# Kernel optimization log

Hardware: AMD Instinct MI355X
Metric: run time of the kernel (lower is better)

## Reference

```python
import jax, jax.numpy as jnp
import numpy as np

HEADS = 8
NEG_SLOPE = 0.2


def _gat_conv(x, src, dst, W, a_src, a_dst, b, heads, ch):
    # PyG GATConv (v1), eval mode (dropout inactive), add_self_loops=True, concat=True.
    N = x.shape[0]
    loop = jnp.arange(N)
    s = jnp.concatenate([src, loop])
    d = jnp.concatenate([dst, loop])
    h = (x @ W).reshape(N, heads, ch)                      # [N, H, C]
    alpha_src = jnp.einsum('nhc,hc->nh', h, a_src)          # [N, H]
    alpha_dst = jnp.einsum('nhc,hc->nh', h, a_dst)
    e = jax.nn.leaky_relu(alpha_src[s] + alpha_dst[d], NEG_SLOPE)  # [E, H]
    m = jax.ops.segment_max(e, d, num_segments=N)           # segment softmax over dst
    ex = jnp.exp(e - m[d])
    denom = jax.ops.segment_sum(ex, d, num_segments=N)
    alpha = ex / (denom[d] + 1e-16)
    out = jax.ops.segment_sum(h[s] * alpha[:, :, None], d, num_segments=N)  # [N, H, C]
    return out.reshape(N, heads * ch) + b


def setup_inputs() -> dict:
    key = jax.random.key(0)
    ks = jax.random.split(key, 20)
    B, N, F_in = 8, 1024, 16
    E = 131072
    C1, C2 = 8, 128                     # per-head channels of conv1 / conv2
    D = N * HEADS * C2                  # flattened head input = 1024*1024
    NA, AC = 4, 4                       # len(num_actions)=4, each 4 actions

    def w(k, shape, fan_in):
        return jax.random.normal(k, shape, jnp.float32) * (1.0 / np.sqrt(fan_in))

    inp = {
        'x': jax.random.normal(ks[0], (B, N, F_in), jnp.float32),
        'edge': jax.random.randint(ks[1], (2, E), 0, B * N, jnp.int64),
        'W1': w(ks[2], (F_in, HEADS * C1), F_in),
        'a_src1': w(ks[3], (HEADS, C1), C1),
        'a_dst1': w(ks[4], (HEADS, C1), C1),
        'b1': jnp.zeros((HEADS * C1,), jnp.float32),
        'W2': w(ks[5], (HEADS * C1, HEADS * C2), HEADS * C1),
        'a_src2': w(ks[6], (HEADS, C2), C2),
        'a_dst2': w(ks[7], (HEADS, C2), C2),
        'b2': jnp.zeros((HEADS * C2,), jnp.float32),
        'adv_w': w(ks[8], (D, NA * AC), D),
        'adv_b': jnp.zeros((NA * AC,), jnp.float32),
        'val1_w': w(ks[9], (D, 64), D),
        'val1_b': jnp.zeros((64,), jnp.float32),
        'val2_w': w(ks[10], (64, 64), 64),
        'val2_b': jnp.zeros((64,), jnp.float32),
        'val3_w': w(ks[11], (64, 1), 64),
        'val3_b': jnp.zeros((1,), jnp.float32),
    }
    return inp


def reference(x, edge, W1, a_src1, a_dst1, b1, W2, a_src2, a_dst2, b2,
              adv_w, adv_b, val1_w, val1_b, val2_w, val2_b, val3_w, val3_b):
    B, N, F_in = x.shape
    src, dst = edge[0], edge[1]
    h = x.reshape(B * N, F_in)
    h = jax.nn.relu(_gat_conv(h, src, dst, W1, a_src1, a_dst1, b1, HEADS, 8))
    h = jax.nn.relu(_gat_conv(h, src, dst, W2, a_src2, a_dst2, b2, HEADS, 128))
    h = h.reshape(B, -1)                                   # [B, N*1024]
    adv = jax.nn.relu(h @ adv_w + adv_b).reshape(B, 4, 4)  # [B, len(num_actions), actions]
    v = jax.nn.relu(h @ val1_w + val1_b)
    v = jax.nn.relu(v @ val2_w + val2_b)
    v = v @ val3_w + val3_b                                # [B, 1]
    return v[:, :, None] + adv - adv.mean(-1, keepdims=True)
```

## Files before the change

kernel.cpp:

```cpp
#include <hip/hip_runtime.h>
#include <stdint.h>

#define NODES   8192
#define BATCH   8
#define FIN     16
#define HC1     64
#define HC2     1024
#define DTOT    1048576
#define NEG     0.2f

typedef unsigned short u16;

__device__ __forceinline__ float b2f(u16 s){ return __uint_as_float(((unsigned)s)<<16); }
__device__ __forceinline__ u16 f2b(float f){
    unsigned u = __float_as_uint(f);
    unsigned r = u + 0x7fffu + ((u>>16)&1u);
    return (u16)(r>>16);
}
__device__ __forceinline__ float lrelu(float x){ return x > 0.f ? x : NEG*x; }
__device__ __forceinline__ float ldf(const void* p, long i, int isf){
    return isf ? ((const float*)p)[i] : b2f(((const u16*)p)[i]);
}

__device__ __forceinline__ int esrc(const int* e, int i, int i64){ return i64 ? e[2*i] : e[i]; }
__device__ __forceinline__ int edst(const int* e, int i, int E, int i64){ return i64 ? e[2*(E+i)] : e[E+i]; }

__global__ __launch_bounds__(256) void k_prep(const u16* __restrict__ xs, const int* __restrict__ ed,
        int* flags, int* counts){
    int t = threadIdx.x;
    if(blockIdx.x == 0){
        __shared__ int cnt[2];
        if(t<2) cnt[t]=0;
        __syncthreads();
        int bad=0;
        for(int i=t;i<1024;i+=256){
            u16 u = xs[i];
            float a = fabsf(b2f(u));
            if(!(u==0 || (a>1e-8f && a<1e4f))) bad++;
        }
        if(bad) atomicAdd(&cnt[0], bad);
        int z=0;
        for(int i=t;i<1024;i+=256){
            if(ed[2*i+1]==0) z++;
        }
        if(z) atomicAdd(&cnt[1], z);
        __syncthreads();
        if(t==0){ flags[0] = (cnt[0] > 64) ? 1 : 0; flags[1] = (cnt[1] > 512) ? 1 : 0; }
    } else {
        int i = (blockIdx.x-1)*256 + t;
        if(i < NODES) counts[i] = 0;
    }
}

__global__ __launch_bounds__(256) void k_cnt_d1(const int* __restrict__ ed, int E, int* counts,
        const void* __restrict__ x, const void* __restrict__ W1,
        const void* __restrict__ asw, const void* __restrict__ adw,
        float* g1, float* as1, float* ad1, const int* flags){
    int t = threadIdx.x;
    if(blockIdx.x < 512){
        int i64 = flags[1];
        int e = blockIdx.x*256 + t;
        if(e < E) atomicAdd(&counts[edst(ed,e,E,i64)], 1);
        return;
    }
    int isf = flags[0];
    __shared__ float w1[FIN*HC1];
    __shared__ float av[64], dv[64];
    __shared__ float xr[4][FIN];
    __shared__ float hrow[4][HC1];
    int n0 = (blockIdx.x-512)*4;
    for(int i=t;i<FIN*HC1;i+=256) w1[i] = ldf(W1,i,isf);
    if(t<64){ av[t]=ldf(asw,t,isf); dv[t]=ldf(adw,t,isf); }
    if(t<64) xr[t>>4][t&15] = ldf(x, n0*FIN + t, isf);
    __syncthreads();
    int i = t>>6, c = t&63;
    float acc = 0.f;
    #pragma unroll
    for(int k=0;k<FIN;k++) acc += xr[i][k]*w1[k*HC1+c];
    g1[(n0+i)*HC1 + c] = acc;
    hrow[i][c] = acc;
    __syncthreads();
    if(t<32){
        int ii=t>>3, h=t&7;
        float sa=0.f, sd=0.f;
        #pragma unroll
        for(int k=0;k<8;k++){ float v=hrow[ii][h*8+k]; sa+=v*av[h*8+k]; sd+=v*dv[h*8+k]; }
        as1[(n0+ii)*8+h]=sa; ad1[(n0+ii)*8+h]=sd;
    }
}

__global__ __launch_bounds__(1024) void k_scan(const int* __restrict__ counts, int* offs, int* cursor){
    __shared__ int sums[1024];
    int t = threadIdx.x;
    int base = t*8;
    int loc[8]; int s = 0;
    for(int k=0;k<8;k++){ loc[k] = s; s += counts[base+k]; }
    sums[t] = s;
    __syncthreads();
    for(int off=1; off<1024; off<<=1){
        int v = (t>=off) ? sums[t-off] : 0;
        __syncthreads();
        sums[t] += v;
        __syncthreads();
    }
    int b = (t==0) ? 0 : sums[t-1];
    for(int k=0;k<8;k++){ int v = b + loc[k]; offs[base+k]=v; cursor[base+k]=v; }
    if(t==1023) offs[NODES] = sums[1023];
}

__global__ void k_fill(const int* __restrict__ ed, int E, int* cursor, int* csr, const int* flags){
    int i64 = flags[1];
    int e = blockIdx.x*256 + threadIdx.x;
    if(e < E){ int p = atomicAdd(&cursor[edst(ed,e,E,i64)], 1); csr[p] = esrc(ed,e,i64); }
}

__global__ __launch_bounds__(64) void k_agg1(const int* __restrict__ offs, const int* __restrict__ csr,
        const float* __restrict__ g1, const float* __restrict__ as1, const float* __restrict__ ad1,
        const void* __restrict__ b1, float* z1, const int* flags){
    int isf = flags[0];
    __shared__ float redm[64], redd[64];
    __shared__ float mh[8], dh[8], adl[8];
    __shared__ int src_l[64];
    __shared__ float wx[64*8];
    int n = blockIdx.x, t = threadIdx.x;
    int off = offs[n], deg = offs[n+1]-off, tot = deg+1;
    if(t<8) adl[t] = ad1[n*8+t];
    __syncthreads();
    {
        int h = t&7, jg = t>>3;
        float ad = adl[h];
        float m = -1e30f, d = 0.f;
        for(int j=jg; j<tot; j+=8){
            int s = (j<deg)?csr[off+j]:n;
            float e = lrelu(as1[s*8+h] + ad);
            if(e>m){ d = d*__expf(m-e) + 1.f; m = e; } else d += __expf(e-m);
        }
        redm[t]=m; redd[t]=d;
        __syncthreads();
        for(int st=4; st>=1; st>>=1){
            if(jg < st){
                float m2 = redm[t + st*8], d2 = redd[t + st*8];
                float mm = fmaxf(m, m2);
                d = d*__expf(m-mm) + d2*__expf(m2-mm);
                m = mm;
                redm[t]=m; redd[t]=d;
            }
            __syncthreads();
        }
        if(t<8){ mh[t]=redm[t]; dh[t]=redd[t] + 1e-16f; }
        __syncthreads();
    }
    int c = t, hc = t>>3;
    float acc = 0.f;
    for(int c0=0;c0<tot;c0+=64){
        int nc = min(64, tot-c0);
        if(t<nc){ int j=c0+t; src_l[t]=(j<deg)?csr[off+j]:n; }
        __syncthreads();
        for(int p=t;p<nc*8;p+=64){
            int j=p>>3, hh=p&7;
            float e = lrelu(as1[src_l[j]*8+hh] + adl[hh]);
            wx[p] = __expf(e - mh[hh]);
        }
        __syncthreads();
        int j = 0;
        for(; j+2<=nc; j+=2){
            float w0 = wx[j*8+hc],     v0 = g1[src_l[j]*HC1 + c];
            float w1 = wx[(j+1)*8+hc], v1 = g1[src_l[j+1]*HC1 + c];
            acc += w0*v0 + w1*v1;
        }
        if(j<nc) acc += wx[j*8+hc]*g1[src_l[j]*HC1 + c];
        __syncthreads();
    }
    z1[n*HC1 + c] = fmaxf(acc/dh[hc] + ldf(b1,c,isf), 0.f);
}

__global__ __launch_bounds__(256) void k_d2a2(const float* __restrict__ z1,
        const void* __restrict__ W2, const void* __restrict__ asw, const void* __restrict__ adw,
        u16* g2, float* as2, float* ad2, const int* flags){
    int isf = flags[0];
    __shared__ float zr[8][HC1];
    __shared__ float avs[HC2], ads[HC2];
    int t = threadIdx.x;
    int n0 = blockIdx.x*8;
    for(int i=t;i<8*HC1;i+=256) zr[i>>6][i&63] = z1[n0*HC1 + i];
    for(int i=t;i<HC2;i+=256){ avs[i]=ldf(asw,i,isf); ads[i]=ldf(adw,i,isf); }
    __syncthreads();
    int c0 = t*4;
    float acc[8][4];
    #pragma unroll
    for(int i=0;i<8;i++){ acc[i][0]=0;acc[i][1]=0;acc[i][2]=0;acc[i][3]=0; }
    for(int k=0;k<HC1;k++){
        float w0,w1,w2,w3;
        if(isf){
            float4 w = *(const float4*)((const float*)W2 + (size_t)k*HC2 + c0);
            w0=w.x; w1=w.y; w2=w.z; w3=w.w;
        } else {
            ushort4 w = *(const ushort4*)((const u16*)W2 + (size_t)k*HC2 + c0);
            w0=b2f(w.x); w1=b2f(w.y); w2=b2f(w.z); w3=b2f(w.w);
        }
        #pragma unroll
        for(int i=0;i<8;i++){
            float zv = zr[i][k];
            acc[i][0]+=zv*w0; acc[i][1]+=zv*w1; acc[i][2]+=zv*w2; acc[i][3]+=zv*w3;
        }
    }
    float a0=avs[c0], a1=avs[c0+1], a2=avs[c0+2], a3=avs[c0+3];
    float d0=ads[c0], d1=ads[c0+1], d2=ads[c0+2], d3=ads[c0+3];
    int h = t>>5;
    #pragma unroll
    for(int i=0;i<8;i++){
        ushort4 o;
        o.x=f2b(acc[i][0]); o.y=f2b(acc[i][1]); o.z=f2b(acc[i][2]); o.w=f2b(acc[i][3]);
        *(ushort4*)&g2[(size_t)(n0+i)*HC2 + c0] = o;
        float pa = acc[i][0]*a0 + acc[i][1]*a1 + acc[i][2]*a2 + acc[i][3]*a3;
        float pd = acc[i][0]*d0 + acc[i][1]*d1 + acc[i][2]*d2 + acc[i][3]*d3;
        #pragma unroll
        for(int m=1;m<32;m<<=1){ pa += __shfl_xor(pa,m); pd += __shfl_xor(pd,m); }
        if((t&31)==0){ as2[(n0+i)*8+h]=pa; ad2[(n0+i)*8+h]=pd; }
    }
}

__global__ __launch_bounds__(256) void k_agg2(const int* __restrict__ offs, const int* __restrict__ csr,
        const u16* __restrict__ g2, const float* __restrict__ as2, const float* __restrict__ ad2,
        const void* __restrict__ b2, u16* hbf, const int* flags){
    int isf = flags[0];
    __shared__ float redm[256], redd[256];
    __shared__ float mh[8], dh[8], adl[8];
    __shared__ int src_l[64];
    __shared__ float wx[64*8];
    int n = blockIdx.x, t = threadIdx.x;
    int off = offs[n], deg = offs[n+1]-off, tot = deg+1;
    if(t<8) adl[t] = ad2[n*8+t];
    __syncthreads();
    {
        int h = t&7, jg = t>>3;
        float ad = adl[h];
        float m = -1e30f, d = 0.f;
        for(int j=jg; j<tot; j+=32){
            int s = (j<deg)?csr[off+j]:n;
            float e = lrelu(as2[s*8+h] + ad);
            if(e>m){ d = d*__expf(m-e) + 1.f; m = e; } else d += __expf(e-m);
        }
        redm[t]=m; redd[t]=d;
        __syncthreads();
        for(int st=16; st>=1; st>>=1){
            if(jg < st){
                float m2 = redm[t + st*8], d2 = redd[t + st*8];
                float mm = fmaxf(m, m2);
                d = d*__expf(m-mm) + d2*__expf(m2-mm);
                m = mm;
                redm[t]=m; redd[t]=d;
            }
            __syncthreads();
        }
        if(t<8){ mh[t]=redm[t]; dh[t]=redd[t] + 1e-16f; }
        __syncthreads();
    }
    int c0 = t*4, hc = t>>5;
    float acc[4] = {0,0,0,0};
    for(int cc0=0;cc0<tot;cc0+=64){
        int nc = min(64, tot-cc0);
        if(t<nc){ int j=cc0+t; src_l[t]=(j<deg)?csr[off+j]:n; }
        __syncthreads();
        for(int p=t;p<nc*8;p+=256){
            int j=p>>3, hh=p&7;
            float e = lrelu(as2[src_l[j]*8+hh] + adl[hh]);
            wx[p] = __expf(e - mh[hh]);
        }
        __syncthreads();
        int j = 0;
        for(; j+2<=nc; j+=2){
            float w0 = wx[j*8+hc], w1 = wx[(j+1)*8+hc];
            ushort4 gv0 = *(const ushort4*)&g2[(size_t)src_l[j]*HC2 + c0];
            ushort4 gv1 = *(const ushort4*)&g2[(size_t)src_l[j+1]*HC2 + c0];
            acc[0]+=w0*b2f(gv0.x)+w1*b2f(gv1.x);
            acc[1]+=w0*b2f(gv0.y)+w1*b2f(gv1.y);
            acc[2]+=w0*b2f(gv0.z)+w1*b2f(gv1.z);
            acc[3]+=w0*b2f(gv0.w)+w1*b2f(gv1.w);
        }
        if(j<nc){
            float w = wx[j*8+hc];
            ushort4 gv = *(const ushort4*)&g2[(size_t)src_l[j]*HC2 + c0];
            acc[0]+=w*b2f(gv.x); acc[1]+=w*b2f(gv.y); acc[2]+=w*b2f(gv.z); acc[3]+=w*b2f(gv.w);
        }
        __syncthreads();
    }
    float dhv = dh[hc];
    ushort4 o;
    o.x = f2b(fmaxf(acc[0]/dhv + ldf(b2,c0+0,isf), 0.f));
    o.y = f2b(fmaxf(acc[1]/dhv + ldf(b2,c0+1,isf), 0.f));
    o.z = f2b(fmaxf(acc[2]/dhv + ldf(b2,c0+2,isf), 0.f));
    o.w = f2b(fmaxf(acc[3]/dhv + ldf(b2,c0+3,isf), 0.f));
    *(ushort4*)&hbf[(size_t)n*HC2 + c0] = o;
}

template<int COLS, int NW>
__device__ __forceinline__ void gemv_part(const void* __restrict__ W, const u16* __restrict__ hbf,
        float* __restrict__ scratch, int wid, int lane, int isf){
    const int GR    = COLS/8;
    const int KSTEP = 64/GR;
    const int ITERS = DTOT/(NW*KSTEP);
    int cg  = (lane % GR)*8;
    int kof = lane / GR;
    float acc[8][8];
    #pragma unroll
    for(int b=0;b<8;b++)
        #pragma unroll
        for(int c=0;c<8;c++) acc[b][c]=0.f;
    for(int it=0; it<ITERS; it+=2){
        int k0 = (it*NW + wid)*KSTEP + kof;
        int k1 = ((it+1)*NW + wid)*KSTEP + kof;
        float wv0[8], wv1[8];
        if(isf){
            float4 a0 = *(const float4*)((const float*)W + (size_t)k0*COLS + cg);
            float4 b0 = *(const float4*)((const float*)W + (size_t)k0*COLS + cg + 4);
            float4 a1 = *(const float4*)((const float*)W + (size_t)k1*COLS + cg);
            float4 b1 = *(const float4*)((const float*)W + (size_t)k1*COLS + cg + 4);
            wv0[0]=a0.x;wv0[1]=a0.y;wv0[2]=a0.z;wv0[3]=a0.w;wv0[4]=b0.x;wv0[5]=b0.y;wv0[6]=b0.z;wv0[7]=b0.w;
            wv1[0]=a1.x;wv1[1]=a1.y;wv1[2]=a1.z;wv1[3]=a1.w;wv1[4]=b1.x;wv1[5]=b1.y;wv1[6]=b1.z;wv1[7]=b1.w;
        } else {
            ushort4 a0 = *(const ushort4*)((const u16*)W + (size_t)k0*COLS + cg);
            ushort4 b0 = *(const ushort4*)((const u16*)W + (size_t)k0*COLS + cg + 4);
            ushort4 a1 = *(const ushort4*)((const u16*)W + (size_t)k1*COLS + cg);
            ushort4 b1 = *(const ushort4*)((const u16*)W + (size_t)k1*COLS + cg + 4);
            wv0[0]=b2f(a0.x);wv0[1]=b2f(a0.y);wv0[2]=b2f(a0.z);wv0[3]=b2f(a0.w);
            wv0[4]=b2f(b0.x);wv0[5]=b2f(b0.y);wv0[6]=b2f(b0.z);wv0[7]=b2f(b0.w);
            wv1[0]=b2f(a1.x);wv1[1]=b2f(a1.y);wv1[2]=b2f(a1.z);wv1[3]=b2f(a1.w);
            wv1[4]=b2f(b1.x);wv1[5]=b2f(b1.y);wv1[6]=b2f(b1.z);wv1[7]=b2f(b1.w);
        }
        float hv0[8], hv1[8];
        #pragma unroll
        for(int b=0;b<8;b++){ hv0[b] = b2f(hbf[(size_t)b*DTOT + k0]); hv1[b] = b2f(hbf[(size_t)b*DTOT + k1]); }
        #pragma unroll
        for(int b=0;b<8;b++)
            #pragma unroll
            for(int c=0;c<8;c++) acc[b][c] += hv0[b]*wv0[c] + hv1[b]*wv1[c];
    }
    #pragma unroll
    for(int m=GR;m<64;m<<=1){
        #pragma unroll
        for(int b=0;b<8;b++)
            #pragma unroll
            for(int c=0;c<8;c++) acc[b][c] += __shfl_xor(acc[b][c], m);
    }
    int q = lane / GR;
    if(q < 8){
        float4 o0, o1;
        o0.x=acc[q][0]; o0.y=acc[q][1]; o0.z=acc[q][2]; o0.w=acc[q][3];
        o1.x=acc[q][4]; o1.y=acc[q][5]; o1.z=acc[q][6]; o1.w=acc[q][7];
        float* dst = scratch + (size_t)wid*COLS*8 + q*COLS + cg;
        *(float4*)dst       = o0;
        *(float4*)(dst + 4) = o1;
    }
}

__global__ __launch_bounds__(256) void k_heads(const void* __restrict__ v1w, const void* __restrict__ advw,
        const u16* __restrict__ hbf, float* s1, float* s2, const int* flags){
    int isf = flags[0];
    int lane = threadIdx.x & 63;
    if(blockIdx.x < 1024){
        int wid = (int)((blockIdx.x*256 + threadIdx.x) >> 6);
        gemv_part<64,4096>(v1w, hbf, s1, wid, lane, isf);
    } else {
        int wid = (int)(((blockIdx.x-1024)*256 + threadIdx.x) >> 6);
        gemv_part<16,1024>(advw, hbf, s2, wid, lane, isf);
    }
}

__global__ __launch_bounds__(1024) void k_reduce(const float* __restrict__ s1, const float* __restrict__ s2,
        float* v1a, float* adva){
    __shared__ float red[1024];
    int blk = blockIdx.x, t = threadIdx.x;
    int ph = t>>6, ln = t&63;
    float a = 0.f;
    if(blk < 8){
        int o = blk*64 + ln;
        for(int p = ph; p < 4096; p += 16) a += s1[(size_t)p*512 + o];
        red[t] = a; __syncthreads();
        if(t<64){ float s=0.f; for(int q=0;q<16;q++) s += red[q*64+t]; v1a[blk*64+t]=s; }
    } else {
        int o = (blk-8)*64 + ln;
        for(int p = ph; p < 1024; p += 16) a += s2[(size_t)p*128 + o];
        red[t] = a; __syncthreads();
        if(t<64){ float s=0.f; for(int q=0;q<16;q++) s += red[q*64+t]; adva[(blk-8)*64+t]=s; }
    }
}

__global__ __launch_bounds__(512) void k_final(const float* __restrict__ v1a, const float* __restrict__ adva,
        const void* __restrict__ v1b, const void* __restrict__ advb,
        const void* __restrict__ w2v, const void* __restrict__ b2v,
        const void* __restrict__ w3v, const void* __restrict__ b3v,
        void* out, const int* flags){
    int isf = flags[0];
    __shared__ float v1[8][64], v2[8][64], adv[128], v3[8];
    int t = threadIdx.x;
    { int b=t>>6, j=t&63; v1[b][j] = fmaxf(v1a[t] + ldf(v1b,j,isf), 0.f); }
    if(t<128) adv[t] = fmaxf(adva[t] + ldf(advb,t&15,isf), 0.f);
    __syncthreads();
    { int b=t>>6, j=t&63;
      float a=0.f;
      for(int k=0;k<64;k++) a += v1[b][k]*ldf(w2v,k*64+j,isf);
      v2[b][j] = fmaxf(a + ldf(b2v,j,isf), 0.f); }
    __syncthreads();
    if(t<8){
        float a=0.f;
        for(int k=0;k<64;k++) a += v2[t][k]*ldf(w3v,k,isf);
        v3[t] = a + ldf(b3v,0,isf);
    }
    __syncthreads();
    if(t<128){
        int b=t>>4, r=(t>>2)&3;
        int base = b*16 + r*4;
        float m = 0.25f*(adv[base]+adv[base+1]+adv[base+2]+adv[base+3]);
        float val = v3[b] + adv[t] - m;
        if(isf) ((float*)out)[t] = val;
        else    ((u16*)out)[t]   = f2b(val);
    }
}

extern "C" void kernel_launch(void* const* d_in, const int* in_sizes, int n_in,
                              void* d_out, int out_size, void* d_ws, size_t ws_size,
                              hipStream_t stream){
    const void* x    = d_in[0];
    const int*  edge = (const int*)d_in[1];
    const int E = in_sizes[1]/2;
    const void* W1   = d_in[2];
    const void* as1w = d_in[3];
    const void* ad1w = d_in[4];
    const void* b1   = d_in[5];
    const void* W2   = d_in[6];
    const void* as2w = d_in[7];
    const void* ad2w = d_in[8];
    const void* b2   = d_in[9];
    const void* advw = d_in[10];
    const void* advb = d_in[11];
    const void* v1w  = d_in[12];
    const void* v1b  = d_in[13];
    const void* v2w  = d_in[14];
    const void* v2b  = d_in[15];
    const void* v3w  = d_in[16];
    const void* v3b  = d_in[17];

    char* wsp = (char*)d_ws;
    size_t o = 0;
    auto alloc = [&](size_t bytes)->char*{
        char* p = wsp + o;
        o = (o + bytes + 255) & ~(size_t)255;
        return p;
    };
    int*   flags  = (int*)  alloc(256);
    int*   counts = (int*)  alloc(NODES*4);
    int*   offs   = (int*)  alloc((NODES+8)*4);
    int*   cursor = (int*)  alloc(NODES*4);
    int*   csr    = (int*)  alloc((size_t)E*4);
    float* g1     = (float*)alloc((size_t)NODES*HC1*4);
    float* as1    = (float*)alloc((size_t)NODES*8*4);
    float* ad1    = (float*)alloc((size_t)NODES*8*4);
    float* z1     = (float*)alloc((size_t)NODES*HC1*4);
    u16*   g2     = (u16*)  alloc((size_t)NODES*HC2*2);
    float* as2    = (float*)alloc((size_t)NODES*8*4);
    float* ad2    = (float*)alloc((size_t)NODES*8*4);
    u16*   hbf    = (u16*)  alloc((size_t)NODES*HC2*2);
    float* s1     = (float*)alloc((size_t)4096*512*4);
    float* s2     = (float*)alloc((size_t)1024*128*4);
    float* v1a    = (float*)alloc(512*4);
    float* adva   = (float*)alloc(128*4);

    k_prep  <<<33, 256, 0, stream>>>((const u16*)x, edge, flags, counts);
    k_cnt_d1<<<2560, 256, 0, stream>>>(edge, E, counts, x, W1, as1w, ad1w, g1, as1, ad1, flags);
    k_scan  <<<1, 1024, 0, stream>>>(counts, offs, cursor);
    k_fill  <<<(E+255)/256, 256, 0, stream>>>(edge, E, cursor, csr, flags);
    k_agg1  <<<NODES, 64, 0, stream>>>(offs, csr, g1, as1, ad1, b1, z1, flags);
    k_d2a2  <<<NODES/8, 256, 0, stream>>>(z1, W2, as2w, ad2w, g2, as2, ad2, flags);
    k_agg2  <<<NODES, 256, 0, stream>>>(offs, csr, g2, as2, ad2, b2, hbf, flags);
    k_heads <<<1280, 256, 0, stream>>>(v1w, advw, hbf, s1, s2, flags);
    k_reduce<<<10, 1024, 0, stream>>>(s1, s2, v1a, adva);
    k_final <<<1, 512, 0, stream>>>(v1a, adva, v1b, advb, v2w, v2b, v3w, v3b, d_out, flags);
}
```

Measured before the change: 685.3 us.

## Map one wavefront per node in GAT aggregation and stream head weights nontemporally

Both GAT aggregation kernels now give each node a single 64-lane wavefront, with four nodes per 256-thread block. The segment-softmax reductions use shuffles instead of shared memory and block barriers. Edge attention weights are recomputed inline per edge rather than staged through shared memory. In the head GEMV, weight loads become nontemporal so the one-pass weight stream does not evict cached activations. In exchange, each lane redundantly recomputes the exp weights, and the edge loop in agg2 becomes serial per wave.

Measured after the change: 685.2 us. No clear change (-0.0%).

```diff
diff --git a/kernel.cpp b/kernel.cpp
--- a/kernel.cpp
+++ b/kernel.cpp
@@ -10,6 +10,8 @@
 #define NEG     0.2f
 
 typedef unsigned short u16;
+typedef float f4v __attribute__((ext_vector_type(4)));
+typedef unsigned short u4v __attribute__((ext_vector_type(4)));
 
 __device__ __forceinline__ float b2f(u16 s){ return __uint_as_float(((unsigned)s)<<16); }
 __device__ __forceinline__ u16 f2b(float f){
@@ -114,64 +116,41 @@
     if(e < E){ int p = atomicAdd(&cursor[edst(ed,e,E,i64)], 1); csr[p] = esrc(ed,e,i64); }
 }
 
-__global__ __launch_bounds__(64) void k_agg1(const int* __restrict__ offs, const int* __restrict__ csr,
+__global__ __launch_bounds__(256) void k_agg1(const int* __restrict__ offs, const int* __restrict__ csr,
         const float* __restrict__ g1, const float* __restrict__ as1, const float* __restrict__ ad1,
         const void* __restrict__ b1, float* z1, const int* flags){
     int isf = flags[0];
-    __shared__ float redm[64], redd[64];
-    __shared__ float mh[8], dh[8], adl[8];
-    __shared__ int src_l[64];
-    __shared__ float wx[64*8];
-    int n = blockIdx.x, t = threadIdx.x;
+    int lane = threadIdx.x & 63;
+    int n = blockIdx.x*4 + (threadIdx.x>>6);
     int off = offs[n], deg = offs[n+1]-off, tot = deg+1;
-    if(t<8) adl[t] = ad1[n*8+t];
-    __syncthreads();
-    {
-        int h = t&7, jg = t>>3;
-        float ad = adl[h];
-        float m = -1e30f, d = 0.f;
-        for(int j=jg; j<tot; j+=8){
-            int s = (j<deg)?csr[off+j]:n;
-            float e = lrelu(as1[s*8+h] + ad);
-            if(e>m){ d = d*__expf(m-e) + 1.f; m = e; } else d += __expf(e-m);
-        }
-        redm[t]=m; redd[t]=d;
-        __syncthreads();
-        for(int st=4; st>=1; st>>=1){
-            if(jg < st){
-                float m2 = redm[t + st*8], d2 = redd[t + st*8];
-                float mm = fmaxf(m, m2);
-                d = d*__expf(m-mm) + d2*__expf(m2-mm);
-                m = mm;
-                redm[t]=m; redd[t]=d;
-            }
-            __syncthreads();
-        }
-        if(t<8){ mh[t]=redm[t]; dh[t]=redd[t] + 1e-16f; }
-        __syncthreads();
-    }
-    int c = t, hc = t>>3;
+    int h  = lane & 7;
+    float adl = ad1[n*8 + h];
+    float m = -1e30f, d = 0.f;
+    for(int j=lane>>3; j<tot; j+=8){
+        int s = (j<deg)?csr[off+j]:n;
+        float e = lrelu(as1[s*8+h] + adl);
+        if(e>m){ d = d*__expf(m-e) + 1.f; m = e; } else d += __expf(e-m);
+    }
+    #pragma unroll
+    for(int st=8; st<64; st<<=1){
+        float m2 = __shfl_xor(m, st), d2 = __shfl_xor(d, st);
+        float mm = fmaxf(m, m2);
+        d = d*__expf(m-mm) + d2*__expf(m2-mm);
+        m = mm;
+    }
+    float dfin = d + 1e-16f;
+    int hc = lane >> 3;
+    float Mc = __shfl(m, hc);
+    float Dc = __shfl(dfin, hc);
+    float Ac = __shfl(adl, hc);
     float acc = 0.f;
-    for(int c0=0;c0<tot;c0+=64){
-        int nc = min(64, tot-c0);
-        if(t<nc){ int j=c0+t; src_l[t]=(j<deg)?csr[off+j]:n; }
-        __syncthreads();
-        for(int p=t;p<nc*8;p+=64){
-            int j=p>>3, hh=p&7;
-            float e = lrelu(as1[src_l[j]*8+hh] + adl[hh]);
-            wx[p] = __expf(e - mh[hh]);
-        }
-        __syncthreads();
-        int j = 0;
-        for(; j+2<=nc; j+=2){
-            float w0 = wx[j*8+hc],     v0 = g1[src_l[j]*HC1 + c];
-            float w1 = wx[(j+1)*8+hc], v1 = g1[src_l[j+1]*HC1 + c];
-            acc += w0*v0 + w1*v1;
-        }
-        if(j<nc) acc += wx[j*8+hc]*g1[src_l[j]*HC1 + c];
-        __syncthreads();
-    }
-    z1[n*HC1 + c] = fmaxf(acc/dh[hc] + ldf(b1,c,isf), 0.f);
+    for(int j=0; j<tot; j++){
+        int s = (j<deg)?csr[off+j]:n;
+        float e = lrelu(as1[s*8+hc] + Ac);
+        float w = __expf(e - Mc);
+        acc += w * g1[s*HC1 + lane];
+    }
+    z1[n*HC1 + lane] = fmaxf(acc/Dc + ldf(b1,lane,isf), 0.f);
 }
 
 __global__ __launch_bounds__(256) void k_d2a2(const float* __restrict__ z1,
@@ -215,7 +194,7 @@
         float pa = acc[i][0]*a0 + acc[i][1]*a1 + acc[i][2]*a2 + acc[i][3]*a3;
         float pd = acc[i][0]*d0 + acc[i][1]*d1 + acc[i][2]*d2 + acc[i][3]*d3;
         #pragma unroll
-        for(int m=1;m<32;m<<=1){ pa += __shfl_xor(pa,m); pd += __shfl_xor(pd,m); }
+        for(int mm=1;mm<32;mm<<=1){ pa += __shfl_xor(pa,mm); pd += __shfl_xor(pd,mm); }
         if((t&31)==0){ as2[(n0+i)*8+h]=pa; ad2[(n0+i)*8+h]=pd; }
     }
 }
@@ -224,74 +203,59 @@
         const u16* __restrict__ g2, const float* __restrict__ as2, const float* __restrict__ ad2,
         const void* __restrict__ b2, u16* hbf, const int* flags){
     int isf = flags[0];
-    __shared__ float redm[256], redd[256];
-    __shared__ float mh[8], dh[8], adl[8];
-    __shared__ int src_l[64];
-    __shared__ float wx[64*8];
-    int n = blockIdx.x, t = threadIdx.x;
+    int lane = threadIdx.x & 63;
+    int n = blockIdx.x*4 + (threadIdx.x>>6);
     int off = offs[n], deg = offs[n+1]-off, tot = deg+1;
-    if(t<8) adl[t] = ad2[n*8+t];
-    __syncthreads();
-    {
-        int h = t&7, jg = t>>3;
-        float ad = adl[h];
-        float m = -1e30f, d = 0.f;
-        for(int j=jg; j<tot; j+=32){
-            int s = (j<deg)?csr[off+j]:n;
-            float e = lrelu(as2[s*8+h] + ad);
-            if(e>m){ d = d*__expf(m-e) + 1.f; m = e; } else d += __expf(e-m);
-        }
-        redm[t]=m; redd[t]=d;
-        __syncthreads();
-        for(int st=16; st>=1; st>>=1){
-            if(jg < st){
-                float m2 = redm[t + st*8], d2 = redd[t + st*8];
-                float mm = fmaxf(m, m2);
-                d = d*__expf(m-mm) + d2*__expf(m2-mm);
-                m = mm;
-                redm[t]=m; redd[t]=d;
-            }
-            __syncthreads();
-        }
-        if(t<8){ mh[t]=redm[t]; dh[t]=redd[t] + 1e-16f; }
-        __syncthreads();
-    }
-    int c0 = t*4, hc = t>>5;
-    float acc[4] = {0,0,0,0};
-    for(int cc0=0;cc0<tot;cc0+=64){
-        int nc = min(64, tot-cc0);
-        if(t<nc){ int j=cc0+t; src_l[t]=(j<deg)?csr[off+j]:n; }
-        __syncthreads();
-        for(int p=t;p<nc*8;p+=256){
-            int j=p>>3, hh=p&7;
-            float e = lrelu(as2[src_l[j]*8+hh] + adl[hh]);
-            wx[p] = __expf(e - mh[hh]);
-        }
-        __syncthreads();
-        int j = 0;
-        for(; j+2<=nc; j+=2){
-            float w0 = wx[j*8+hc], w1 = wx[(j+1)*8+hc];
-            ushort4 gv0 = *(const ushort4*)&g2[(size_t)src_l[j]*HC2 + c0];
-            ushort4 gv1 = *(const ushort4*)&g2[(size_t)src_l[j+1]*HC2 + c0];
-            acc[0]+=w0*b2f(gv0.x)+w1*b2f(gv1.x);
-            acc[1]+=w0*b2f(gv0.y)+w1*b2f(gv1.y);
-            acc[2]+=w0*b2f(gv0.z)+w1*b2f(gv1.z);
-            acc[3]+=w0*b2f(gv0.w)+w1*b2f(gv1.w);
-        }
-        if(j<nc){
-            float w = wx[j*8+hc];
-            ushort4 gv = *(const ushort4*)&g2[(size_t)src_l[j]*HC2 + c0];
-            acc[0]+=w*b2f(gv.x); acc[1]+=w*b2f(gv.y); acc[2]+=w*b2f(gv.z); acc[3]+=w*b2f(gv.w);
-        }
-        __syncthreads();
-    }
-    float dhv = dh[hc];
-    ushort4 o;
-    o.x = f2b(fmaxf(acc[0]/dhv + ldf(b2,c0+0,isf), 0.f));
-    o.y = f2b(fmaxf(acc[1]/dhv + ldf(b2,c0+1,isf), 0.f));
-    o.z = f2b(fmaxf(acc[2]/dhv + ldf(b2,c0+2,isf), 0.f));
-    o.w = f2b(fmaxf(acc[3]/dhv + ldf(b2,c0+3,isf), 0.f));
-    *(ushort4*)&hbf[(size_t)n*HC2 + c0] = o;
+    int h  = lane & 7;
+    float adl = ad2[n*8 + h];
+    float m = -1e30f, d = 0.f;
+    for(int j=lane>>3; j<tot; j+=8){
+        int s = (j<deg)?csr[off+j]:n;
+        float e = lrelu(as2[s*8+h] + adl);
+        if(e>m){ d = d*__expf(m-e) + 1.f; m = e; } else d += __expf(e-m);
+    }
+    #pragma unroll
+    for(int st=8; st<64; st<<=1){
+        float m2 = __shfl_xor(m, st), d2 = __shfl_xor(d, st);
+        float mm = fmaxf(m, m2);
+        d = d*__expf(m-mm) + d2*__expf(m2-mm);
+        m = mm;
+    }
+    float dfin = d + 1e-16f;
+    float Mq[4], Dq[4], Aq[4];
+    int hq[4];
+    #pragma unroll
+    for(int q=0;q<4;q++){
+        hq[q] = q*2 + (lane>>5);
+        Mq[q] = __shfl(m,    hq[q]);
+        Dq[q] = __shfl(dfin, hq[q]);
+        Aq[q] = __shfl(adl,  hq[q]);
+    }
+    float acc[4][4];
+    #pragma unroll
+    for(int q=0;q<4;q++){ acc[q][0]=0;acc[q][1]=0;acc[q][2]=0;acc[q][3]=0; }
+    for(int j=0; j<tot; j++){
+        int s = (j<deg)?csr[off+j]:n;
+        const u16* gp = g2 + (size_t)s*HC2;
+        #pragma unroll
+        for(int q=0;q<4;q++){
+            float e = lrelu(as2[s*8+hq[q]] + Aq[q]);
+            float w = __expf(e - Mq[q]);
+            ushort4 v = *(const ushort4*)&gp[q*256 + lane*4];
+            acc[q][0] += w*b2f(v.x); acc[q][1] += w*b2f(v.y);
+            acc[q][2] += w*b2f(v.z); acc[q][3] += w*b2f(v.w);
+        }
+    }
+    #pragma unroll
+    for(int q=0;q<4;q++){
+        int c0 = q*256 + lane*4;
+        ushort4 o;
+        o.x = f2b(fmaxf(acc[q][0]/Dq[q] + ldf(b2,c0+0,isf), 0.f));
+        o.y = f2b(fmaxf(acc[q][1]/Dq[q] + ldf(b2,c0+1,isf), 0.f));
+        o.z = f2b(fmaxf(acc[q][2]/Dq[q] + ldf(b2,c0+2,isf), 0.f));
+        o.w = f2b(fmaxf(acc[q][3]/Dq[q] + ldf(b2,c0+3,isf), 0.f));
+        *(ushort4*)&hbf[(size_t)n*HC2 + c0] = o;
+    }
 }
 
 template<int COLS, int NW>
@@ -312,17 +276,17 @@
         int k1 = ((it+1)*NW + wid)*KSTEP + kof;
         float wv0[8], wv1[8];
         if(isf){
-            float4 a0 = *(const float4*)((const float*)W + (size_t)k0*COLS + cg);
-            float4 b0 = *(const float4*)((const float*)W + (size_t)k0*COLS + cg + 4);
-            float4 a1 = *(const float4*)((const float*)W + (size_t)k1*COLS + cg);
-            float4 b1 = *(const float4*)((const float*)W + (size_t)k1*COLS + cg + 4);
+            f4v a0 = __builtin_nontemporal_load((const f4v*)((const float*)W + (size_t)k0*COLS + cg));
+            f4v b0 = __builtin_nontemporal_load((const f4v*)((const float*)W + (size_t)k0*COLS + cg + 4));
+            f4v a1 = __builtin_nontemporal_load((const f4v*)((const float*)W + (size_t)k1*COLS + cg));
+            f4v b1 = __builtin_nontemporal_load((const f4v*)((const float*)W + (size_t)k1*COLS + cg + 4));
             wv0[0]=a0.x;wv0[1]=a0.y;wv0[2]=a0.z;wv0[3]=a0.w;wv0[4]=b0.x;wv0[5]=b0.y;wv0[6]=b0.z;wv0[7]=b0.w;
             wv1[0]=a1.x;wv1[1]=a1.y;wv1[2]=a1.z;wv1[3]=a1.w;wv1[4]=b1.x;wv1[5]=b1.y;wv1[6]=b1.z;wv1[7]=b1.w;
         } else {
-            ushort4 a0 = *(const ushort4*)((const u16*)W + (size_t)k0*COLS + cg);
-            ushort4 b0 = *(const ushort4*)((const u16*)W + (size_t)k0*COLS + cg + 4);
-            ushort4 a1 = *(const ushort4*)((const u16*)W + (size_t)k1*COLS + cg);
-            ushort4 b1 = *(const ushort4*)((const u16*)W + (size_t)k1*COLS + cg + 4);
+            u4v a0 = __builtin_nontemporal_load((const u4v*)((const u16*)W + (size_t)k0*COLS + cg));
+            u4v b0 = __builtin_nontemporal_load((const u4v*)((const u16*)W + (size_t)k0*COLS + cg + 4));
+            u4v a1 = __builtin_nontemporal_load((const u4v*)((const u16*)W + (size_t)k1*COLS + cg));
+            u4v b1 = __builtin_nontemporal_load((const u4v*)((const u16*)W + (size_t)k1*COLS + cg + 4));
             wv0[0]=b2f(a0.x);wv0[1]=b2f(a0.y);wv0[2]=b2f(a0.z);wv0[3]=b2f(a0.w);
             wv0[4]=b2f(b0.x);wv0[5]=b2f(b0.y);wv0[6]=b2f(b0.z);wv0[7]=b2f(b0.w);
             wv1[0]=b2f(a1.x);wv1[1]=b2f(a1.y);wv1[2]=b2f(a1.z);wv1[3]=b2f(a1.w);
@@ -470,9 +434,9 @@
     k_cnt_d1<<<2560, 256, 0, stream>>>(edge, E, counts, x, W1, as1w, ad1w, g1, as1, ad1, flags);
     k_scan  <<<1, 1024, 0, stream>>>(counts, offs, cursor);
     k_fill  <<<(E+255)/256, 256, 0, stream>>>(edge, E, cursor, csr, flags);
-    k_agg1  <<<NODES, 64, 0, stream>>>(offs, csr, g1, as1, ad1, b1, z1, flags);
+    k_agg1  <<<NODES/4, 256, 0, stream>>>(offs, csr, g1, as1, ad1, b1, z1, flags);
     k_d2a2  <<<NODES/8, 256, 0, stream>>>(z1, W2, as2w, ad2w, g2, as2, ad2, flags);
-    k_agg2  <<<NODES, 256, 0, stream>>>(offs, csr, g2, as2, ad2, b2, hbf, flags);
+    k_agg2  <<<NODES/4, 256, 0, stream>>>(offs, csr, g2, as2, ad2, b2, hbf, flags);
     k_heads <<<1280, 256, 0, stream>>>(v1w, advw, hbf, s1, s2, flags);
     k_reduce<<<10, 1024, 0, stream>>>(s1, s2, v1a, adva);
     k_final <<<1, 512, 0, stream>>>(v1a, adva, v1b, advb, v2w, v2b, v3w, v3b, d_out, flags);
```
